# Kernel optimization log

Hardware: AMD Instinct MI355X
Metric: run time of the kernel (lower is better)

## Reference

```python
import jax, jax.numpy as jnp
import numpy as np

B, N, C, H, DEPTH, MLP = 8, 1024, 768, 12, 8, 3072
HD = C // H
SCALE = HD ** -0.5
EPS = 1e-5


def layer_norm(x, g, b):
    mu = jnp.mean(x, -1, keepdims=True)
    var = jnp.mean((x - mu) ** 2, -1, keepdims=True)
    return (x - mu) / jnp.sqrt(var + EPS) * g + b


def setup_inputs() -> dict:
    key = jax.random.key(0)
    ks = jax.random.split(key, 8)
    s = 0.02
    return {
        "x": jax.random.normal(ks[0], (B, N, C), jnp.float32),
        "ln1_g": jnp.ones((DEPTH, C), jnp.float32),
        "ln1_b": jnp.zeros((DEPTH, C), jnp.float32),
        "wqkv": jax.random.normal(ks[1], (DEPTH, C, 3 * C), jnp.float32) * s,
        "wproj": jax.random.normal(ks[2], (DEPTH, C, C), jnp.float32) * s,
        "bproj": jnp.zeros((DEPTH, C), jnp.float32),
        "ln2_g": jnp.ones((DEPTH, C), jnp.float32),
        "ln2_b": jnp.zeros((DEPTH, C), jnp.float32),
        "w1": jax.random.normal(ks[3], (DEPTH, C, MLP), jnp.float32) * s,
        "b1": jnp.zeros((DEPTH, MLP), jnp.float32),
        "w2": jax.random.normal(ks[4], (DEPTH, MLP, C), jnp.float32) * s,
        "b2": jnp.zeros((DEPTH, C), jnp.float32),
    }


def reference(x, ln1_g, ln1_b, wqkv, wproj, bproj, ln2_g, ln2_b, w1, b1, w2, b2):
    def body(h, p):
        g1, be1, wq, wp, bp, g2, be2, wf1, bf1, wf2, bf2 = p
        # --- attention block: Residual(PreNorm(SelfAttention)) ---
        y = layer_norm(h, g1, be1)
        qkv = (y @ wq).reshape(B, N, 3, H, HD)
        qkv = jnp.transpose(qkv, (2, 0, 3, 1, 4))  # [3, B, H, N, HD]
        q, k, v = qkv[0], qkv[1], qkv[2]
        logits = jnp.einsum("bhnd,bhmd->bhnm", q, k) * SCALE
        # source applies softmax twice (faithful to original)
        attn = jax.nn.softmax(jax.nn.softmax(logits, axis=-1), axis=-1)
        o = jnp.einsum("bhnm,bhmd->bhnd", attn, v)
        o = jnp.transpose(o, (0, 2, 1, 3)).reshape(B, N, C)
        h = h + o @ wp + bp
        # --- FFN block: Residual(PreNorm(FeedForward)) ---
        y2 = layer_norm(h, g2, be2)
        f = jax.nn.relu(y2 @ wf1 + bf1) @ wf2 + bf2
        return h + f, None

    out, _ = jax.lax.scan(body, x, (ln1_g, ln1_b, wqkv, wproj, bproj, ln2_g, ln2_b, w1, b1, w2, b2))
    return out
```

## Files before the change

### kernel.cpp

```cpp
#include <hip/hip_runtime.h>
#include <hip/hip_bf16.h>

#define DEPTHL 8
#define BZ 8
#define SEQ 1024
#define CDIM 768
#define HEADS 12
#define HDIM 64
#define MLPD 3072
#define TOK (BZ*SEQ)
#define QKVN (3*CDIM)

typedef __attribute__((ext_vector_type(8))) short vshort8;
typedef __attribute__((ext_vector_type(4))) short vshort4;
typedef __attribute__((ext_vector_type(4))) float vfloat4;

__device__ __forceinline__ short bf16_bits(float f) {
  union { float f; unsigned u; } x; x.f = f;
  unsigned r = (x.u + 0x7FFFu + ((x.u >> 16) & 1u)) >> 16;
  return (short)r;
}

__device__ __forceinline__ unsigned pk_bf16(float a, float b) {
  unsigned r;
  asm("v_cvt_pk_bf16_f32 %0, %1, %2" : "=v"(r) : "v"(a), "v"(b));
  return r;
}

#define GL16(g, l) __builtin_amdgcn_global_load_lds( \
    (const __attribute__((address_space(1))) unsigned int*)(g), \
    (__attribute__((address_space(3))) unsigned int*)(l), 16, 0, 0)

__global__ __launch_bounds__(256) void wconv_t(const float* __restrict__ in,
                                               short* __restrict__ out,
                                               int K, int N) {
  __shared__ float tile[32][33];
  const long d = blockIdx.z;
  in  += d * (long)K * N;
  out += d * (long)N * K;
  const int n0 = blockIdx.x * 32, k0 = blockIdx.y * 32;
  const int tx = threadIdx.x & 31, ty = threadIdx.x >> 5;
#pragma unroll
  for (int i = 0; i < 4; i++)
    tile[ty + 8*i][tx] = in[(long)(k0 + ty + 8*i) * N + n0 + tx];
  __syncthreads();
#pragma unroll
  for (int i = 0; i < 4; i++)
    out[(long)(n0 + ty + 8*i) * K + k0 + tx] = bf16_bits(tile[tx][ty + 8*i]);
}

__global__ __launch_bounds__(256) void vtrans(const short* __restrict__ qkv,
                                              short* __restrict__ vt) {
  __shared__ short tile[32][34];
  const int bh = blockIdx.z;
  const int b = bh / HEADS, hh = bh % HEADS;
  const int t0 = blockIdx.x * 32, d0 = blockIdx.y * 32;
  const int tx = threadIdx.x & 31, ty = threadIdx.x >> 5;
  const short* src = qkv + ((long)b * SEQ + t0) * QKVN + 2 * CDIM + hh * HDIM + d0;
#pragma unroll
  for (int i = 0; i < 4; i++)
    tile[ty + 8*i][tx] = src[(long)(ty + 8*i) * QKVN + tx];
  __syncthreads();
  short* dst = vt + (long)bh * HDIM * SEQ + (long)d0 * SEQ + t0;
#pragma unroll
  for (int i = 0; i < 4; i++)
    dst[(long)(ty + 8*i) * SEQ + tx] = tile[tx][ty + 8*i];
}

__global__ __launch_bounds__(192) void ln_fwd(const float* __restrict__ h,
                                              const float* __restrict__ g,
                                              const float* __restrict__ be,
                                              short* __restrict__ y) {
  __shared__ float red[3];
  const int row = blockIdx.x;
  const int tid = threadIdx.x;
  const float4 v = ((const float4*)(h + (long)row * CDIM))[tid];
  float s = v.x + v.y + v.z + v.w;
#pragma unroll
  for (int m = 32; m >= 1; m >>= 1) s += __shfl_xor(s, m);
  if ((tid & 63) == 0) red[tid >> 6] = s;
  __syncthreads();
  const float mu = (red[0] + red[1] + red[2]) * (1.0f / CDIM);
  float dx = v.x - mu, dy = v.y - mu, dz = v.z - mu, dw = v.w - mu;
  float q = dx*dx + dy*dy + dz*dz + dw*dw;
  __syncthreads();
#pragma unroll
  for (int m = 32; m >= 1; m >>= 1) q += __shfl_xor(q, m);
  if ((tid & 63) == 0) red[tid >> 6] = q;
  __syncthreads();
  const float rstd = rsqrtf((red[0] + red[1] + red[2]) * (1.0f / CDIM) + 1e-5f);
  const float4 g4 = ((const float4*)g)[tid];
  const float4 b4 = ((const float4*)be)[tid];
  vshort4 o;
  o[0] = bf16_bits(dx * rstd * g4.x + b4.x);
  o[1] = bf16_bits(dy * rstd * g4.y + b4.y);
  o[2] = bf16_bits(dz * rstd * g4.z + b4.z);
  o[3] = bf16_bits(dw * rstd * g4.w + b4.w);
  *(vshort4*)(y + (long)row * CDIM + tid * 4) = o;
}

template<int EPI>
__global__ __launch_bounds__(256) void gemm_bt(const short* __restrict__ A,
                                               const short* __restrict__ Bt,
                                               const float* __restrict__ bias,
                                               void* __restrict__ Cout,
                                               int M, int N, int K) {
  __shared__ short As[128 * 32];
  __shared__ short Bs[128 * 32];
  const int tid = threadIdx.x;
  const int wid = tid >> 6, lane = tid & 63;
  const int lg = lane >> 4, lr = lane & 15;
  const int wm = wid >> 1, wn = wid & 1;

  const int gx = gridDim.x;
  const int nwg = gx * gridDim.y;
  int flat = blockIdx.y * gx + blockIdx.x;
  flat = (flat & 7) * (nwg >> 3) + (flat >> 3);
  const long bx = flat % gx;
  const long by = flat / gx;

  vfloat4 acc[4][4];
#pragma unroll
  for (int i = 0; i < 4; i++)
#pragma unroll
    for (int j = 0; j < 4; j++) acc[i][j] = (vfloat4){0.f, 0.f, 0.f, 0.f};

  const int c = wid * 64 + lane;
  const short* Ag0 = A  + (by * 128 +      (c >> 2)) * (long)K + (c & 3) * 8;
  const short* Ag1 = A  + (by * 128 + 64 + (c >> 2)) * (long)K + (c & 3) * 8;
  const short* Bg0 = Bt + (bx * 128 +      (c >> 2)) * (long)K + (c & 3) * 8;
  const short* Bg1 = Bt + (bx * 128 + 64 + (c >> 2)) * (long)K + (c & 3) * 8;
  short* Al = As + c * 8;
  short* Bl = Bs + c * 8;

  for (int kk = 0; kk < K; kk += 32) {
    __syncthreads();
    GL16(Ag0 + kk, Al);
    GL16(Ag1 + kk, Al + 2048);
    GL16(Bg0 + kk, Bl);
    GL16(Bg1 + kk, Bl + 2048);
    __syncthreads();
    vshort8 a[4], b[4];
#pragma unroll
    for (int mt = 0; mt < 4; mt++)
      a[mt] = *(const vshort8*)(As + (wm * 64 + mt * 16 + lr) * 32 + lg * 8);
#pragma unroll
    for (int nt = 0; nt < 4; nt++)
      b[nt] = *(const vshort8*)(Bs + (wn * 64 + nt * 16 + lr) * 32 + lg * 8);
#pragma unroll
    for (int mt = 0; mt < 4; mt++)
#pragma unroll
      for (int nt = 0; nt < 4; nt++)
        acc[mt][nt] = __builtin_amdgcn_mfma_f32_16x16x32_bf16(a[mt], b[nt], acc[mt][nt], 0, 0, 0);
  }

  const long row0 = by * 128 + wm * 64;
  const long col0 = bx * 128 + wn * 64;
#pragma unroll
  for (int mt = 0; mt < 4; mt++) {
#pragma unroll
    for (int nt = 0; nt < 4; nt++) {
      const long col = col0 + nt * 16 + lr;
      float bv = 0.f;
      if (EPI != 0) bv = bias[col];
#pragma unroll
      for (int r = 0; r < 4; r++) {
        const long row = row0 + mt * 16 + lg * 4 + r;
        float v = acc[mt][nt][r];
        if (EPI == 0) {
          ((short*)Cout)[row * N + col] = bf16_bits(v);
        } else if (EPI == 1) {
          v += bv; v = v > 0.f ? v : 0.f;
          ((short*)Cout)[row * N + col] = bf16_bits(v);
        } else {
          float* hp = (float*)Cout + row * N + col;
          *hp = *hp + v + bv;
        }
      }
    }
  }
}

__global__ __launch_bounds__(256, 4) void attn_fused4(const short* __restrict__ qkv,
                                                      const short* __restrict__ vt,
                                                      short* __restrict__ o) {
  __shared__ __align__(16) short P_lds[4 * 4096];
  __shared__ float redm[4][16], redz[4][16], redt[4][16];
  int flat = blockIdx.y * 64 + blockIdx.x;
  flat = (flat & 7) * (6144 >> 3) + (flat >> 3);
  const int qt = flat & 63;
  const int bh = flat >> 6;
  const int b = bh / HEADS, hh = bh % HEADS;
  const int tid = threadIdx.x, wid = tid >> 6, lane = tid & 63;
  const int lg = lane >> 4, lr = lane & 15;
  const long tokbase = (long)b * SEQ;
  const short* qbase = qkv + tokbase * QKVN + hh * HDIM;
  const short* kbase = qkv + tokbase * QKVN + CDIM + hh * HDIM;
  const short* vtb = vt + (long)bh * HDIM * SEQ;
  char* Pw = (char*)P_lds + wid * 8192;

  vshort8 qf[2];
#pragma unroll
  for (int ks = 0; ks < 2; ks++)
    qf[ks] = *(const vshort8*)(qbase + (long)(qt * 16 + lr) * QKVN + ks * 32 + lg * 8);

  vfloat4 s[16];
#pragma unroll
  for (int bb = 0; bb < 4; bb++) {
    vshort8 kf[8];
#pragma unroll
    for (int u = 0; u < 4; u++) {
      const int n0 = wid * 256 + (bb * 4 + u) * 16;
#pragma unroll
      for (int ks = 0; ks < 2; ks++)
        kf[u * 2 + ks] = *(const vshort8*)(kbase + (long)(n0 + lr) * QKVN + ks * 32 + lg * 8);
    }
#pragma unroll
    for (int u = 0; u < 4; u++) {
      vfloat4 acc = (vfloat4){0.f, 0.f, 0.f, 0.f};
      acc = __builtin_amdgcn_mfma_f32_16x16x32_bf16(kf[u * 2 + 0], qf[0], acc, 0, 0, 0);
      acc = __builtin_amdgcn_mfma_f32_16x16x32_bf16(kf[u * 2 + 1], qf[1], acc, 0, 0, 0);
      s[bb * 4 + u] = acc;
    }
  }

  float mt16[16];
#pragma unroll
  for (int i = 0; i < 16; i++)
    mt16[i] = fmaxf(fmaxf(s[i][0], s[i][1]), fmaxf(s[i][2], s[i][3]));
#pragma unroll
  for (int st = 8; st >= 1; st >>= 1)
#pragma unroll
    for (int i = 0; i < 8; i++) if (i < st) mt16[i] = fmaxf(mt16[i], mt16[i + st]);
  float m = mt16[0];
  m = fmaxf(m, __shfl_xor(m, 16));
  m = fmaxf(m, __shfl_xor(m, 32));
  if (lane < 16) redm[wid][lr] = m;
  __syncthreads();
  m = fmaxf(fmaxf(redm[0][lr], redm[1][lr]), fmaxf(redm[2][lr], redm[3][lr]));
  const float msc = m * 0.125f;

  float zt[16];
#pragma unroll
  for (int i = 0; i < 16; i++) {
    float e0 = __expf(fmaf(s[i][0], 0.125f, -msc));
    float e1 = __expf(fmaf(s[i][1], 0.125f, -msc));
    float e2 = __expf(fmaf(s[i][2], 0.125f, -msc));
    float e3 = __expf(fmaf(s[i][3], 0.125f, -msc));
    s[i][0] = e0; s[i][1] = e1; s[i][2] = e2; s[i][3] = e3;
    zt[i] = (e0 + e1) + (e2 + e3);
  }
#pragma unroll
  for (int st = 8; st >= 1; st >>= 1)
#pragma unroll
    for (int i = 0; i < 8; i++) if (i < st) zt[i] += zt[i + st];
  float z = zt[0];
  z += __shfl_xor(z, 16);
  z += __shfl_xor(z, 32);
  if (lane < 16) redz[wid][lr] = z;
  __syncthreads();
  z = (redz[0][lr] + redz[1][lr]) + (redz[2][lr] + redz[3][lr]);
  const float rz = 1.0f / z;

  float tt[16];
#pragma unroll
  for (int i = 0; i < 16; i++) {
    float p0 = __expf(s[i][0] * rz);
    float p1 = __expf(s[i][1] * rz);
    float p2 = __expf(s[i][2] * rz);
    float p3 = __expf(s[i][3] * rz);
    s[i][0] = p0; s[i][1] = p1; s[i][2] = p2; s[i][3] = p3;
    tt[i] = (p0 + p1) + (p2 + p3);
  }
#pragma unroll
  for (int st = 8; st >= 1; st >>= 1)
#pragma unroll
    for (int i = 0; i < 8; i++) if (i < st) tt[i] += tt[i + st];
  float t2 = tt[0];
  t2 += __shfl_xor(t2, 16);
  t2 += __shfl_xor(t2, 32);
  if (lane < 16) redt[wid][lr] = t2;
  __syncthreads();
  t2 = (redt[0][lr] + redt[1][lr]) + (redt[2][lr] + redt[3][lr]);
  const float rt = 1.0f / t2;

#pragma unroll
  for (int i = 0; i < 16; i++) {
    const int byt = (lr * 512 + i * 32 + lg * 8) ^ ((lr & 7) << 4);
    uint2 pk;
    pk.x = pk_bf16(s[i][0] * rt, s[i][1] * rt);
    pk.y = pk_bf16(s[i][2] * rt, s[i][3] * rt);
    *(uint2*)(Pw + byt) = pk;
  }

  vfloat4 oacc[4];
#pragma unroll
  for (int dt = 0; dt < 4; dt++) oacc[dt] = (vfloat4){0.f, 0.f, 0.f, 0.f};
#pragma unroll
  for (int j = 0; j < 8; j++) {
    const int abyt = (lr * 512 + j * 64 + lg * 16) ^ ((lr & 7) << 4);
    vshort8 af = *(const vshort8*)(Pw + abyt);
#pragma unroll
    for (int dt = 0; dt < 4; dt++) {
      vshort8 vb = *(const vshort8*)(vtb + (long)(dt * 16 + lr) * SEQ + wid * 256 + j * 32 + lg * 8);
      oacc[dt] = __builtin_amdgcn_mfma_f32_16x16x32_bf16(af, vb, oacc[dt], 0, 0, 0);
    }
  }

#pragma unroll
  for (int dt = 0; dt < 4; dt++)
#pragma unroll
    for (int r = 0; r < 4; r++)
      *(float*)(Pw + ((lg * 4 + r) * 64 + dt * 16 + lr) * 4) = oacc[dt][r];
  __syncthreads();

  const int q = tid >> 4, d0 = (tid & 15) * 4;
  float4 a0 = *(const float4*)((const char*)P_lds + 0 * 8192 + (q * 64 + d0) * 4);
  float4 a1 = *(const float4*)((const char*)P_lds + 1 * 8192 + (q * 64 + d0) * 4);
  float4 a2 = *(const float4*)((const char*)P_lds + 2 * 8192 + (q * 64 + d0) * 4);
  float4 a3 = *(const float4*)((const char*)P_lds + 3 * 8192 + (q * 64 + d0) * 4);
  float ox = (a0.x + a1.x) + (a2.x + a3.x);
  float oy = (a0.y + a1.y) + (a2.y + a3.y);
  float oz = (a0.z + a1.z) + (a2.z + a3.z);
  float ow = (a0.w + a1.w) + (a2.w + a3.w);
  uint2 ob;
  ob.x = pk_bf16(ox, oy);
  ob.y = pk_bf16(oz, ow);
  *(uint2*)(o + (tokbase + qt * 16 + q) * CDIM + hh * HDIM + d0) = ob;
}

extern "C" void kernel_launch(void* const* d_in, const int* in_sizes, int n_in,
                              void* d_out, int out_size, void* d_ws, size_t ws_size,
                              hipStream_t stream) {
  const float* x     = (const float*)d_in[0];
  const float* ln1_g = (const float*)d_in[1];
  const float* ln1_b = (const float*)d_in[2];
  const float* wqkv  = (const float*)d_in[3];
  const float* wproj = (const float*)d_in[4];
  const float* bproj = (const float*)d_in[5];
  const float* ln2_g = (const float*)d_in[6];
  const float* ln2_b = (const float*)d_in[7];
  const float* w1    = (const float*)d_in[8];
  const float* b1    = (const float*)d_in[9];
  const float* w2    = (const float*)d_in[10];
  const float* b2    = (const float*)d_in[11];
  float* h = (float*)d_out;

  char* ws = (char*)d_ws;
  short* wqkv_t  = (short*)ws; ws += (size_t)DEPTHL * QKVN * CDIM * 2;
  short* wproj_t = (short*)ws; ws += (size_t)DEPTHL * CDIM * CDIM * 2;
  short* w1_t    = (short*)ws; ws += (size_t)DEPTHL * MLPD * CDIM * 2;
  short* w2_t    = (short*)ws; ws += (size_t)DEPTHL * CDIM * MLPD * 2;
  short* ybf     = (short*)ws; ws += (size_t)TOK * CDIM * 2;
  short* qkvbf   = (short*)ws; ws += (size_t)TOK * QKVN * 2;
  short* obf     = (short*)ws; ws += (size_t)TOK * CDIM * 2;
  short* f1bf    = (short*)ws; ws += (size_t)TOK * MLPD * 2;
  short* vtb     = f1bf;

  hipMemcpyAsync(h, x, (size_t)TOK * CDIM * sizeof(float), hipMemcpyDeviceToDevice, stream);

  wconv_t<<<dim3(QKVN / 32, CDIM / 32, DEPTHL), 256, 0, stream>>>(wqkv, wqkv_t, CDIM, QKVN);
  wconv_t<<<dim3(CDIM / 32, CDIM / 32, DEPTHL), 256, 0, stream>>>(wproj, wproj_t, CDIM, CDIM);
  wconv_t<<<dim3(MLPD / 32, CDIM / 32, DEPTHL), 256, 0, stream>>>(w1, w1_t, CDIM, MLPD);
  wconv_t<<<dim3(CDIM / 32, MLPD / 32, DEPTHL), 256, 0, stream>>>(w2, w2_t, MLPD, CDIM);

  for (int l = 0; l < DEPTHL; l++) {
    ln_fwd<<<TOK, 192, 0, stream>>>(h, ln1_g + l * CDIM, ln1_b + l * CDIM, ybf);
    gemm_bt<0><<<dim3(QKVN / 128, TOK / 128), 256, 0, stream>>>(
        ybf, wqkv_t + (size_t)l * QKVN * CDIM, nullptr, qkvbf, TOK, QKVN, CDIM);
    vtrans<<<dim3(SEQ / 32, HDIM / 32, BZ * HEADS), 256, 0, stream>>>(qkvbf, vtb);
    attn_fused4<<<dim3(SEQ / 16, BZ * HEADS), 256, 0, stream>>>(qkvbf, vtb, obf);
    gemm_bt<2><<<dim3(CDIM / 128, TOK / 128), 256, 0, stream>>>(
        obf, wproj_t + (size_t)l * CDIM * CDIM, bproj + l * CDIM, h, TOK, CDIM, CDIM);
    ln_fwd<<<TOK, 192, 0, stream>>>(h, ln2_g + l * CDIM, ln2_b + l * CDIM, ybf);
    gemm_bt<1><<<dim3(MLPD / 128, TOK / 128), 256, 0, stream>>>(
        ybf, w1_t + (size_t)l * MLPD * CDIM, b1 + l * MLPD, f1bf, TOK, MLPD, CDIM);
    gemm_bt<2><<<dim3(CDIM / 128, TOK / 128), 256, 0, stream>>>(
        f1bf, w2_t + (size_t)l * CDIM * MLPD, b2 + l * CDIM, h, TOK, CDIM, MLPD);
  }
}
```

Before: 3.508 ms.

## Add 256x256-tile 8-wave pipelined GEMM for QKV and FC1 projections

Adds a new GEMM kernel with 256x256 output tiles, 8 waves per block, and a 4-stage LDS ring with XOR-swizzled direct global-to-LDS loads. It interleaves A/B staging with two MFMA phases, uses a workgroup remap for L2 locality, and raises priority during the MFMA bursts. The QKV and FC1 GEMMs now use it. The goal is more data reuse per tile and better overlap of loads with math, at the cost of more registers and LDS, fewer blocks (QKV gets 9x32 blocks), and the risk of poor wave balance on the smaller grid.

After: 3.530 ms. About the same (+0.7%).

```diff
diff --git a/kernel.cpp b/kernel.cpp
--- a/kernel.cpp
+++ b/kernel.cpp
@@ -167,6 +167,146 @@
       for (int r = 0; r < 4; r++) {
         const long row = row0 + mt * 16 + lg * 4 + r;
         float v = acc[mt][nt][r];
+        if (EPI == 0) {
+          ((short*)Cout)[row * N + col] = bf16_bits(v);
+        } else if (EPI == 1) {
+          v += bv; v = v > 0.f ? v : 0.f;
+          ((short*)Cout)[row * N + col] = bf16_bits(v);
+        } else {
+          float* hp = (float*)Cout + row * N + col;
+          *hp = *hp + v + bv;
+        }
+      }
+    }
+  }
+}
+
+template<int EPI>
+__global__ __launch_bounds__(512, 2) void gemm8(const short* __restrict__ A,
+                                                const short* __restrict__ Bt,
+                                                const float* __restrict__ bias,
+                                                void* __restrict__ Cout,
+                                                int M, int N, int K) {
+  __shared__ short lds[8 * 8192];
+  const int tid = threadIdx.x;
+  const int lane = tid & 63;
+  const int wid = tid >> 6;
+  const int lg = lane >> 4, lr = lane & 15;
+  const int wr = wid >> 2, wn = wid & 3;
+
+  const int gx = gridDim.x, nwg = gx * gridDim.y;
+  int flat = blockIdx.y * gx + blockIdx.x;
+  flat = (flat & 7) * (nwg >> 3) + (flat >> 3);
+  const long bx = flat % gx, by = flat / gx;
+
+  const int NT = K >> 5;
+
+  vfloat4 acc[8][4];
+#pragma unroll
+  for (int i = 0; i < 8; i++)
+#pragma unroll
+    for (int j = 0; j < 4; j++) acc[i][j] = (vfloat4){0.f, 0.f, 0.f, 0.f};
+
+  auto STAGE_A = [&](int kt) {
+    const int buf = kt & 3;
+#pragma unroll
+    for (int ch = 0; ch < 2; ++ch) {
+      const int dst = tid * 16 + ch * 8192;
+      const int off = dst ^ (((dst >> 7) & 7) << 4);
+      const short* src = A + (by * 256 + (off >> 6)) * (long)K + kt * 32 + ((off & 63) >> 1);
+      GL16(src, lds + ((buf * 2 + 0) << 13) + (dst >> 1));
+    }
+  };
+  auto STAGE_B = [&](int kt) {
+    const int buf = kt & 3;
+#pragma unroll
+    for (int ch = 0; ch < 2; ++ch) {
+      const int dst = tid * 16 + ch * 8192;
+      const int off = dst ^ (((dst >> 7) & 7) << 4);
+      const short* src = Bt + (bx * 256 + (off >> 6)) * (long)K + kt * 32 + ((off & 63) >> 1);
+      GL16(src, lds + ((buf * 2 + 1) << 13) + (dst >> 1));
+    }
+  };
+
+  STAGE_A(0); STAGE_B(0);
+  STAGE_A(1); STAGE_B(1);
+  STAGE_A(2); STAGE_B(2);
+  asm volatile("s_waitcnt vmcnt(8)" ::: "memory");
+  __builtin_amdgcn_sched_barrier(0);
+  __builtin_amdgcn_s_barrier();
+
+  for (int T = 0; T < NT; ++T) {
+    const int buf = T & 3;
+    const int abase = (buf * 2 + 0) << 14;
+    const int bbase = (buf * 2 + 1) << 14;
+    vshort8 a[4], b[4];
+
+#pragma unroll
+    for (int mf = 0; mf < 4; ++mf) {
+      int byt = (wr * 128 + mf * 16 + lr) * 64 + lg * 16;
+      byt ^= ((byt >> 7) & 7) << 4;
+      a[mf] = *(const vshort8*)((const char*)lds + abase + byt);
+    }
+#pragma unroll
+    for (int nf = 0; nf < 4; ++nf) {
+      int byt = (wn * 64 + nf * 16 + lr) * 64 + lg * 16;
+      byt ^= ((byt >> 7) & 7) << 4;
+      b[nf] = *(const vshort8*)((const char*)lds + bbase + byt);
+    }
+    if (T + 3 < NT) STAGE_A(T + 3);
+    __builtin_amdgcn_s_barrier();
+    asm volatile("s_waitcnt lgkmcnt(0)" ::: "memory");
+    __builtin_amdgcn_sched_barrier(0);
+    __builtin_amdgcn_s_setprio(1);
+#pragma unroll
+    for (int mf = 0; mf < 4; ++mf)
+#pragma unroll
+      for (int nf = 0; nf < 4; ++nf)
+        acc[mf][nf] = __builtin_amdgcn_mfma_f32_16x16x32_bf16(a[mf], b[nf], acc[mf][nf], 0, 0, 0);
+    __builtin_amdgcn_s_setprio(0);
+    __builtin_amdgcn_s_barrier();
+
+    vshort8 a2[4];
+#pragma unroll
+    for (int mf = 0; mf < 4; ++mf) {
+      int byt = (wr * 128 + (4 + mf) * 16 + lr) * 64 + lg * 16;
+      byt ^= ((byt >> 7) & 7) << 4;
+      a2[mf] = *(const vshort8*)((const char*)lds + abase + byt);
+    }
+    if (T + 3 < NT) STAGE_B(T + 3);
+    __builtin_amdgcn_s_barrier();
+    asm volatile("s_waitcnt lgkmcnt(0)" ::: "memory");
+    __builtin_amdgcn_sched_barrier(0);
+    __builtin_amdgcn_s_setprio(1);
+#pragma unroll
+    for (int mf = 0; mf < 4; ++mf)
+#pragma unroll
+      for (int nf = 0; nf < 4; ++nf)
+        acc[4 + mf][nf] = __builtin_amdgcn_mfma_f32_16x16x32_bf16(a2[mf], b[nf], acc[4 + mf][nf], 0, 0, 0);
+    __builtin_amdgcn_s_setprio(0);
+    if (T < NT - 2) {
+      asm volatile("s_waitcnt vmcnt(4)" ::: "memory");
+      __builtin_amdgcn_sched_barrier(0);
+    } else if (T == NT - 2) {
+      asm volatile("s_waitcnt vmcnt(0)" ::: "memory");
+      __builtin_amdgcn_sched_barrier(0);
+    }
+    __builtin_amdgcn_s_barrier();
+  }
+
+  const long row0 = by * 256 + wr * 128;
+  const long col0 = bx * 256 + wn * 64;
+#pragma unroll
+  for (int mf = 0; mf < 8; ++mf) {
+#pragma unroll
+    for (int nf = 0; nf < 4; ++nf) {
+      const long col = col0 + nf * 16 + lr;
+      float bv = 0.f;
+      if (EPI != 0) bv = bias[col];
+#pragma unroll
+      for (int r = 0; r < 4; ++r) {
+        const long row = row0 + mf * 16 + lg * 4 + r;
+        float v = acc[mf][nf][r];
         if (EPI == 0) {
           ((short*)Cout)[row * N + col] = bf16_bits(v);
         } else if (EPI == 1) {
@@ -366,14 +506,14 @@
 
   for (int l = 0; l < DEPTHL; l++) {
     ln_fwd<<<TOK, 192, 0, stream>>>(h, ln1_g + l * CDIM, ln1_b + l * CDIM, ybf);
-    gemm_bt<0><<<dim3(QKVN / 128, TOK / 128), 256, 0, stream>>>(
+    gemm8<0><<<dim3(QKVN / 256, TOK / 256), 512, 0, stream>>>(
         ybf, wqkv_t + (size_t)l * QKVN * CDIM, nullptr, qkvbf, TOK, QKVN, CDIM);
     vtrans<<<dim3(SEQ / 32, HDIM / 32, BZ * HEADS), 256, 0, stream>>>(qkvbf, vtb);
     attn_fused4<<<dim3(SEQ / 16, BZ * HEADS), 256, 0, stream>>>(qkvbf, vtb, obf);
     gemm_bt<2><<<dim3(CDIM / 128, TOK / 128), 256, 0, stream>>>(
         obf, wproj_t + (size_t)l * CDIM * CDIM, bproj + l * CDIM, h, TOK, CDIM, CDIM);
     ln_fwd<<<TOK, 192, 0, stream>>>(h, ln2_g + l * CDIM, ln2_b + l * CDIM, ybf);
-    gemm_bt<1><<<dim3(MLPD / 128, TOK / 128), 256, 0, stream>>>(
+    gemm8<1><<<dim3(MLPD / 256, TOK / 256), 512, 0, stream>>>(
         ybf, w1_t + (size_t)l * MLPD * CDIM, b1 + l * MLPD, f1bf, TOK, MLPD, CDIM);
     gemm_bt<2><<<dim3(CDIM / 128, TOK / 128), 256, 0, stream>>>(
         f1bf, w2_t + (size_t)l * CDIM * MLPD, b2 + l * CDIM, h, TOK, CDIM, MLPD);
```

## Double GEMM K-tile to 64 and XOR-swizzle LDS layout to avoid bank conflicts

Applied to the files above, without the earlier changes.

The bf16 GEMM kernel now stages a 128x64 K-slice per iteration instead of 128x32, which halves the number of barrier pairs per K loop. It also applies an XOR swizzle on 16-byte chunks, both when the global-to-LDS copy writes and when the MFMA fragments are read back. The intent is to cut synchronization overhead and LDS bank conflicts on the fragment loads. In exchange it doubles shared memory per block to 32 KB, which may reduce occupancy.

Measured after the change: 3.314 ms. -5.5%, faster.

```diff
diff --git a/kernel.cpp b/kernel.cpp
--- a/kernel.cpp
+++ b/kernel.cpp
@@ -105,8 +105,8 @@
                                                const float* __restrict__ bias,
                                                void* __restrict__ Cout,
                                                int M, int N, int K) {
-  __shared__ short As[128 * 32];
-  __shared__ short Bs[128 * 32];
+  __shared__ short As[128 * 64];
+  __shared__ short Bs[128 * 64];
   const int tid = threadIdx.x;
   const int wid = tid >> 6, lane = tid & 63;
   const int lg = lane >> 4, lr = lane & 15;
@@ -125,33 +125,44 @@
 #pragma unroll
     for (int j = 0; j < 4; j++) acc[i][j] = (vfloat4){0.f, 0.f, 0.f, 0.f};
 
-  const int c = wid * 64 + lane;
-  const short* Ag0 = A  + (by * 128 +      (c >> 2)) * (long)K + (c & 3) * 8;
-  const short* Ag1 = A  + (by * 128 + 64 + (c >> 2)) * (long)K + (c & 3) * 8;
-  const short* Bg0 = Bt + (bx * 128 +      (c >> 2)) * (long)K + (c & 3) * 8;
-  const short* Bg1 = Bt + (bx * 128 + 64 + (c >> 2)) * (long)K + (c & 3) * 8;
-  short* Al = As + c * 8;
-  short* Bl = Bs + c * 8;
-
-  for (int kk = 0; kk < K; kk += 32) {
+  const short* Abase = A  + by * 128 * (long)K;
+  const short* Bbase = Bt + bx * 128 * (long)K;
+
+  for (int kk = 0; kk < K; kk += 64) {
     __syncthreads();
-    GL16(Ag0 + kk, Al);
-    GL16(Ag1 + kk, Al + 2048);
-    GL16(Bg0 + kk, Bl);
-    GL16(Bg1 + kk, Bl + 2048);
+#pragma unroll
+    for (int ch = 0; ch < 4; ch++) {
+      const int dst = tid * 16 + ch * 4096;
+      const int off = dst ^ (((dst >> 7) & 7) << 4);
+      const long srow = off >> 7;
+      const int scol = (off & 127) >> 1;
+      GL16(Abase + srow * K + kk + scol, As + (dst >> 1));
+      GL16(Bbase + srow * K + kk + scol, Bs + (dst >> 1));
+    }
     __syncthreads();
-    vshort8 a[4], b[4];
-#pragma unroll
-    for (int mt = 0; mt < 4; mt++)
-      a[mt] = *(const vshort8*)(As + (wm * 64 + mt * 16 + lr) * 32 + lg * 8);
-#pragma unroll
-    for (int nt = 0; nt < 4; nt++)
-      b[nt] = *(const vshort8*)(Bs + (wn * 64 + nt * 16 + lr) * 32 + lg * 8);
-#pragma unroll
-    for (int mt = 0; mt < 4; mt++)
-#pragma unroll
-      for (int nt = 0; nt < 4; nt++)
-        acc[mt][nt] = __builtin_amdgcn_mfma_f32_16x16x32_bf16(a[mt], b[nt], acc[mt][nt], 0, 0, 0);
+#pragma unroll
+    for (int kh = 0; kh < 2; kh++) {
+      vshort8 a[4], b[4];
+#pragma unroll
+      for (int mt = 0; mt < 4; mt++) {
+        const int row = wm * 64 + mt * 16 + lr;
+        int byt = row * 128 + kh * 64 + lg * 16;
+        byt ^= (row & 7) << 4;
+        a[mt] = *(const vshort8*)((const char*)As + byt);
+      }
+#pragma unroll
+      for (int nt = 0; nt < 4; nt++) {
+        const int row = wn * 64 + nt * 16 + lr;
+        int byt = row * 128 + kh * 64 + lg * 16;
+        byt ^= (row & 7) << 4;
+        b[nt] = *(const vshort8*)((const char*)Bs + byt);
+      }
+#pragma unroll
+      for (int mt = 0; mt < 4; mt++)
+#pragma unroll
+        for (int nt = 0; nt < 4; nt++)
+          acc[mt][nt] = __builtin_amdgcn_mfma_f32_16x16x32_bf16(a[mt], b[nt], acc[mt][nt], 0, 0, 0);
+    }
   }
 
   const long row0 = by * 128 + wm * 64;
```
